# Optimization experiments

Hardware: AMD Instinct MI355X
Metric: run time of the kernel (lower is better)

Reference implementation:

```python
import jax, jax.numpy as jnp
import numpy as np

V, C, L, D = 16384, 16, 6, 64  # n_vars, max_clauses, max_variables, embedding_dim


def _normalize(x):
    # utils.normalize: L2-normalize along the feature axis
    return x / jnp.linalg.norm(x, axis=-1, keepdims=True)


def _rescombine(x, W1, b1, W2, b2):
    # ResidualCombine: normalize(sigmoid(layer1(x)) + layer2(x))
    h = jax.nn.sigmoid(x @ W1 + b1) + x @ W2 + b2
    return _normalize(h)


def setup_inputs() -> dict:
    key = jax.random.key(0)
    ks = jax.random.split(key, 14)
    s = 0.05
    variables = jax.random.normal(ks[0], (V, D), jnp.float32)
    # literal variable indices; slot 0 of every clause is the owning variable i
    lits = jax.random.randint(ks[1], (V, C, L), 0, V)
    lits = lits.at[:, :, 0].set(jnp.arange(V)[:, None])
    neg_mask = jax.random.bernoulli(ks[2], 0.5, (V, C, L))
    # literal validity: at least 2 literals per clause, slot 0 always valid
    nvar = jax.random.randint(ks[3], (V, C), 2, L + 1)
    var_valid = jnp.arange(L)[None, None, :] < nvar[:, :, None]
    # clause validity: at least 1 clause per variable
    nclause = jax.random.randint(ks[4], (V,), 1, C + 1)
    clause_valid = jnp.arange(C)[None, :] < nclause[:, None]
    # params
    Wn = jax.random.normal(ks[5], (D, D), jnp.float32) * s
    bn = jnp.zeros((D,), jnp.float32)
    f = jax.random.normal(ks[6], (D,), jnp.float32)
    false_emb = f / jnp.linalg.norm(f)  # Embedding(1, D, max_norm=1.0)
    W1v = jax.random.normal(ks[7], (L * D, D), jnp.float32) * s
    b1v = jnp.zeros((D,), jnp.float32)
    W2v = jax.random.normal(ks[8], (L * D, D), jnp.float32) * s
    b2v = jnp.zeros((D,), jnp.float32)
    W1c = jax.random.normal(ks[9], (C * D, D), jnp.float32) * s
    b1c = jnp.zeros((D,), jnp.float32)
    W2c = jax.random.normal(ks[10], (C * D, D), jnp.float32) * s
    b2c = jnp.zeros((D,), jnp.float32)
    return dict(variables=variables, lits=lits, neg_mask=neg_mask, var_valid=var_valid,
                clause_valid=clause_valid, Wn=Wn, bn=bn, false_emb=false_emb,
                W1v=W1v, b1v=b1v, W2v=W2v, b2v=b2v, W1c=W1c, b1c=b1c, W2c=W2c, b2c=b2c)


def reference(variables, lits, neg_mask, var_valid, clause_valid,
              Wn, bn, false_emb, W1v, b1v, W2v, b2v, W1c, b1c, W2c, b2c):
    # gather literal embeddings: [V, C, L, D]
    g = variables[lits]
    # negation linear for negative literals
    v = jnp.where(neg_mask[..., None], g @ Wn + bn, g)
    # pad invalid literal slots with the 'false' embedding
    v = jnp.where(var_valid[..., None], v, false_emb)
    # variable_combiner over flattened [L*D]
    clause_emb = _rescombine(v.reshape(V, C, L * D), W1v, b1v, W2v, b2v)  # [V, C, D]
    # pad missing clauses with 'true' = negation(false)
    true_emb = false_emb @ Wn + bn
    clause_emb = jnp.where(clause_valid[..., None], clause_emb, true_emb)
    # clause_combiner over flattened [C*D]
    out = _rescombine(clause_emb.reshape(V, C * D), W1c, b1c, W2c, b2c)  # [V, D]
    # variables with no clauses pass through unchanged
    has_clauses = clause_valid.any(axis=-1)
    return jnp.where(has_clauses[:, None], out, variables)
```

## Files before the change

kernel.cpp:

```cpp
#include <hip/hip_runtime.h>
#include <hip/hip_bf16.h>

#define NV 16384
#define NC 16
#define NL 6
#define ND 64

typedef unsigned short u16;
typedef unsigned int u32;
typedef __attribute__((ext_vector_type(8))) short short8;
typedef __attribute__((ext_vector_type(4))) float f32x4;

#define PB_BN  0
#define PB_FE  64
#define PB_B1V 128
#define PB_B2V 192
#define PB_B1C 256
#define PB_B2C 320
#define U_BVS   896
#define U_BCS   50048
#define U_BN    181120
#define U_VARSB 185216
#define U_NEGB  1233856
#define U_FIDX  2282496

__device__ __forceinline__ float ldbf(const u16* p, int i) {
  return __uint_as_float(((u32)p[i]) << 16);
}
__device__ __forceinline__ u16 f2b(float f) {
  u32 x = __float_as_uint(f);
  return (u16)((x + 0x7FFF + ((x >> 16) & 1)) >> 16);
}
__device__ __forceinline__ int ldmask(const void* p, int i, int bdt) {
  return bdt ? (int)((const signed char*)p)[i] : ((const int*)p)[i];
}
__device__ __forceinline__ float ldf(const void* p, int i, int fdt) {
  return fdt ? ldbf((const u16*)p, i) : ((const float*)p)[i];
}
__device__ __forceinline__ void gll16(const u16* g, u16* l) {
  __builtin_amdgcn_global_load_lds(
      (const __attribute__((address_space(1))) u32*)(g),
      (__attribute__((address_space(3))) u32*)(l), 16, 0, 0);
}

__global__ __launch_bounds__(256) void k_prep(
    const void* vars, const int* __restrict__ lits, const void* negm, const void* vval,
    const void* Wn, const void* bn, const void* femb,
    const void* W1v, const void* b1v, const void* W2v, const void* b2v,
    const void* W1c, const void* b1c, const void* W2c, const void* b2c,
    int* flags, float* pbuf, u16* wsB) {
  __shared__ int s_cnt[4], s_big[4];
  const int t = threadIdx.x;
  {
    const u32 w = ((const u32*)vars)[t];
    const u32 e = (w >> 7) & 0xFF;
    const unsigned long long bal = __ballot(e >= 0x6E && e <= 0x8E);
    const u32 bw = ((const u32*)vval)[t];
    const unsigned long long bb = __ballot(bw > 1u);
    if ((t & 63) == 0) { s_cnt[t >> 6] = __popcll(bal); s_big[t >> 6] = (bb != 0ull); }
  }
  __syncthreads();
  const int fdt = (s_cnt[0] + s_cnt[1] + s_cnt[2] + s_cnt[3]) >= 192;
  const int bdt = (s_big[0] | s_big[1] | s_big[2] | s_big[3]);
  const int bid = blockIdx.x;

  if (bid == 0) {
    if (t == 0) { flags[0] = fdt; flags[1] = bdt; }
    if (t < 64) {
      const void* src[6] = {bn, femb, b1v, b2v, b1c, b2c};
      const int off[6] = {PB_BN, PB_FE, PB_B1V, PB_B2V, PB_B1C, PB_B2C};
      for (int j = 0; j < 6; j++) pbuf[off[j] + t] = ldf(src[j], t, fdt);
      wsB[U_VARSB + NV * 64 + t] = fdt ? ((const u16*)femb)[t] : f2b(((const float*)femb)[t]);
    }
    for (int i = t; i < 4096; i += 256) {
      const int n = i >> 6, k = i & 63;
      wsB[U_BN + i] = f2b(ldf(Wn, k * 64 + n, fdt));
    }
  } else if (bid < 25) {
    const int c = (bid - 1) * 256 + t;
    const int ln = c & 63, nt = (c >> 6) & 7, ks = c >> 9;
    const int n = nt * 16 + (ln & 15);
    const void* src = (n < 64) ? W1v : W2v;
    const int kb = ks * 32 + (ln >> 4) * 8, n6 = n & 63;
    u16 o[8];
#pragma unroll
    for (int j = 0; j < 8; j++) o[j] = f2b(ldf(src, (kb + j) * 64 + n6, fdt));
    *(short8*)(wsB + U_BVS + c * 8) = *(short8*)o;
  } else if (bid < 89) {
    const int c = (bid - 25) * 256 + t;
    const int ln = c & 63, nt = (c >> 6) & 7, ks = c >> 9;
    const int n = nt * 16 + (ln & 15);
    const void* src = (n < 64) ? W1c : W2c;
    const int kb = ks * 32 + (ln >> 4) * 8, n6 = n & 63;
    u16 o[8];
#pragma unroll
    for (int j = 0; j < 8; j++) o[j] = f2b(ldf(src, (kb + j) * 64 + n6, fdt));
    *(short8*)(wsB + U_BCS + c * 8) = *(short8*)o;
  } else if (bid < 601) {
    const int c8 = (bid - 89) * 256 + t;
    u16 o[8];
    if (fdt) {
      *(short8*)o = ((const short8*)vars)[c8];
    } else {
      const float* f = (const float*)vars + c8 * 8;
#pragma unroll
      for (int j = 0; j < 8; j++) o[j] = f2b(f[j]);
    }
    *(short8*)(wsB + U_VARSB + c8 * 8) = *(short8*)o;
  } else {
    const int i0 = ((bid - 601) * 256 + t) * 4;
    u16 o[4];
#pragma unroll
    for (int j = 0; j < 4; j++) {
      const int i = i0 + j;
      const int valid = ldmask(vval, i, bdt);
      const int neg = ldmask(negm, i, bdt);
      const int idx = lits[i];
      o[j] = (u16)(valid ? (idx + (neg ? (NV + 1) : 0)) : NV);
    }
    *(ushort4*)(wsB + U_FIDX + i0) = *(ushort4*)o;
  }
}

__global__ __launch_bounds__(256) void k_negvar(const float* pbuf, u16* wsB) {
  const int tid = threadIdx.x, lane = tid & 63, wv = tid >> 6;
  const int col = lane & 15, quad = lane >> 4, q8 = quad * 8;
  const int rowbase = blockIdx.x * 64 + wv * 16;
  f32x4 acc[4];
#pragma unroll
  for (int nt = 0; nt < 4; nt++) acc[nt] = (f32x4){0.f, 0.f, 0.f, 0.f};
  const int arow = min(rowbase + col, NV);
#pragma unroll
  for (int ks = 0; ks < 2; ks++) {
    const short8 a = *(const short8*)(wsB + U_VARSB + arow * 64 + ks * 32 + q8);
#pragma unroll
    for (int nt = 0; nt < 4; nt++) {
      const short8 b = *(const short8*)(wsB + U_BN + (nt * 16 + col) * 64 + ks * 32 + q8);
      acc[nt] = __builtin_amdgcn_mfma_f32_16x16x32_bf16(a, b, acc[nt], 0, 0, 0);
    }
  }
#pragma unroll
  for (int reg = 0; reg < 4; reg++) {
    const int r = rowbase + quad * 4 + reg;
    if (r <= NV) {
#pragma unroll
      for (int nt = 0; nt < 4; nt++) {
        const int d = nt * 16 + col;
        wsB[U_NEGB + r * 64 + d] = f2b(acc[nt][reg] + pbuf[PB_BN + d]);
      }
    }
  }
}

__global__ __launch_bounds__(256, 2) void k_main(
    const void* __restrict__ vars, const void* __restrict__ cval,
    const float* __restrict__ pbuf, const int* __restrict__ flags,
    const u16* __restrict__ wsB, void* __restrict__ outv) {
  __shared__ __align__(16) u16 smem[24576];
  __shared__ float ps[16][4];
  __shared__ int hcS[16];

  const int tid = threadIdx.x, lane = tid & 63, wv = tid >> 6;
  const int col = lane & 15, quad = lane >> 4, q8 = quad * 8;
  const int fdt = flags[0], bdt = flags[1];
  const int vbase = (blockIdx.x * 4 + wv) * 4;
  const int v0 = blockIdx.x * 16;

  u32 r2_[4][3];
#pragma unroll
  for (int v4 = 0; v4 < 4; v4++)
#pragma unroll
    for (int i = 0; i < 3; i++)
      r2_[v4][i] = *(const u32*)(wsB + U_FIDX + (vbase + v4) * 96 + col * 6 + i * 2);

  const int cv = ldmask(cval, vbase * 16 + lane, bdt);
  const unsigned long long bal = __ballot(cv != 0);
  if (lane < 4) hcS[wv * 4 + lane] = ((bal >> (lane * 16)) & 0xFFFFull) != 0;

  f32x4 acc[4][8];
#pragma unroll
  for (int v4 = 0; v4 < 4; v4++)
#pragma unroll
    for (int nt = 0; nt < 8; nt++) acc[v4][nt] = (f32x4){0.f, 0.f, 0.f, 0.f};

#pragma unroll
  for (int j = 0; j < 6; j++) {
    const int cl = wv * 6 + j;
    gll16(wsB + U_BVS + cl * 512 + lane * 8, &smem[cl * 512]);
  }
  short8 a_cur[4], a_nxt[4];
#pragma unroll
  for (int v4 = 0; v4 < 4; v4++) {
    const int idx = (int)(r2_[v4][0] & 0xFFFFu);
    a_cur[v4] = *(const short8*)(wsB + U_VARSB + idx * 64 + q8);
  }
  __syncthreads();

  for (int q = 0; q < 4; q++) {
    if (q < 3) {
#pragma unroll
      for (int j = 0; j < 6; j++) {
        const int cl = wv * 6 + j;
        gll16(wsB + U_BVS + (q + 1) * 12288 + cl * 512 + lane * 8,
              &smem[((q + 1) & 1) * 12288 + cl * 512]);
      }
    }
#pragma unroll
    for (int ksl = 0; ksl < 3; ksl++) {
      const int gk = q * 3 + ksl;
      if (gk < 11) {
        const int gn = gk + 1;
        const int goff = (gn & 1) * 32 + q8;
        const int pi = gn >> 2, ph = (gn >> 1) & 1;
#pragma unroll
        for (int v4 = 0; v4 < 4; v4++) {
          const int idx = (int)((r2_[v4][pi] >> (ph * 16)) & 0xFFFFu);
          a_nxt[v4] = *(const short8*)(wsB + U_VARSB + idx * 64 + goff);
        }
      }
#pragma unroll
      for (int nt = 0; nt < 8; nt++) {
        const short8 b = *(const short8*)(&smem[(q & 1) * 12288 + (ksl * 8 + nt) * 512 + lane * 8]);
#pragma unroll
        for (int v4 = 0; v4 < 4; v4++)
          acc[v4][nt] = __builtin_amdgcn_mfma_f32_16x16x32_bf16(a_cur[v4], b, acc[v4][nt], 0, 0, 0);
      }
#pragma unroll
      for (int v4 = 0; v4 < 4; v4++) a_cur[v4] = a_nxt[v4];
    }
    if (q < 3) __syncthreads();
  }
  __syncthreads();

  {
    float b1l[4], b2l[4], truel[4];
#pragma unroll
    for (int nt = 0; nt < 4; nt++) {
      const int d = nt * 16 + col;
      b1l[nt] = pbuf[PB_B1V + d];
      b2l[nt] = pbuf[PB_B2V + d];
      truel[nt] = ldbf(wsB, U_NEGB + NV * 64 + d);
    }
#pragma unroll
    for (int v4 = 0; v4 < 4; v4++) {
      const u32 vmask = (u32)((bal >> (v4 * 16)) & 0xFFFFull);
      const int vloc = wv * 4 + v4;
#pragma unroll
      for (int reg = 0; reg < 4; reg++) {
        const int c = quad * 4 + reg;
        float hh[4], ss = 0.f;
#pragma unroll
        for (int nt = 0; nt < 4; nt++) {
          hh[nt] = 1.0f / (1.0f + __expf(-(acc[v4][nt][reg] + b1l[nt]))) + acc[v4][nt + 4][reg] + b2l[nt];
          ss += hh[nt] * hh[nt];
        }
        ss += __shfl_xor(ss, 1, 64); ss += __shfl_xor(ss, 2, 64);
        ss += __shfl_xor(ss, 4, 64); ss += __shfl_xor(ss, 8, 64);
        const float sc = 1.0f / sqrtf(ss);
        const int valid = (vmask >> c) & 1;
#pragma unroll
        for (int nt = 0; nt < 4; nt++) {
          const float o = valid ? hh[nt] * sc : truel[nt];
          const int l2 = (nt * 2 + (col >> 3)) & 3;
          smem[(c * 2 + (nt >> 1)) * 512 + (l2 * 16 + vloc) * 8 + (col & 7)] = f2b(o);
        }
      }
    }
  }
  __syncthreads();

  f32x4 acc1 = (f32x4){0.f, 0.f, 0.f, 0.f}, acc2 = (f32x4){0.f, 0.f, 0.f, 0.f};
#pragma unroll 8
  for (int ks = 0; ks < 32; ks++) {
    const short8 a = *(const short8*)(&smem[ks * 512 + lane * 8]);
    const short8 b1 = *(const short8*)(wsB + U_BCS + (ks * 8 + wv) * 512 + lane * 8);
    const short8 b2 = *(const short8*)(wsB + U_BCS + (ks * 8 + wv + 4) * 512 + lane * 8);
    acc1 = __builtin_amdgcn_mfma_f32_16x16x32_bf16(a, b1, acc1, 0, 0, 0);
    acc2 = __builtin_amdgcn_mfma_f32_16x16x32_bf16(a, b2, acc2, 0, 0, 0);
  }

  const int d = wv * 16 + col;
  const float b1c_d = pbuf[PB_B1C + d], b2c_d = pbuf[PB_B2C + d];
  float h[4];
#pragma unroll
  for (int reg = 0; reg < 4; reg++) {
    h[reg] = 1.0f / (1.0f + __expf(-(acc1[reg] + b1c_d))) + acc2[reg] + b2c_d;
    float ssp = h[reg] * h[reg];
    ssp += __shfl_xor(ssp, 1, 64); ssp += __shfl_xor(ssp, 2, 64);
    ssp += __shfl_xor(ssp, 4, 64); ssp += __shfl_xor(ssp, 8, 64);
    if (col == 0) ps[quad * 4 + reg][wv] = ssp;
  }
  __syncthreads();
#pragma unroll
  for (int reg = 0; reg < 4; reg++) {
    const int r = quad * 4 + reg;
    const float tot = ps[r][0] + ps[r][1] + ps[r][2] + ps[r][3];
    float o = h[reg] * (1.0f / sqrtf(tot));
    const int oi = (v0 + r) * 64 + d;
    if (hcS[r]) {
      if (fdt) ((u16*)outv)[oi] = f2b(o);
      else ((float*)outv)[oi] = o;
    } else {
      if (fdt) ((u16*)outv)[oi] = ((const u16*)vars)[oi];
      else ((float*)outv)[oi] = ((const float*)vars)[oi];
    }
  }
}

extern "C" void kernel_launch(void* const* d_in, const int* in_sizes, int n_in,
                              void* d_out, int out_size, void* d_ws, size_t ws_size,
                              hipStream_t stream) {
  const void* vars = d_in[0];
  const int* lits = (const int*)d_in[1];
  const void* negm = d_in[2];
  const void* vval = d_in[3];
  const void* cvalid = d_in[4];
  const void* Wn = d_in[5];
  const void* bn = d_in[6];
  const void* femb = d_in[7];
  const void* W1v = d_in[8];
  const void* b1v = d_in[9];
  const void* W2v = d_in[10];
  const void* b2v = d_in[11];
  const void* W1c = d_in[12];
  const void* b1c = d_in[13];
  const void* W2c = d_in[14];
  const void* b2c = d_in[15];

  int* flags = (int*)d_ws;
  float* pbuf = (float*)((char*)d_ws + 256);
  u16* wsB = (u16*)d_ws;

  k_prep<<<2137, 256, 0, stream>>>(vars, lits, negm, vval, Wn, bn, femb,
                                   W1v, b1v, W2v, b2v, W1c, b1c, W2c, b2c,
                                   flags, pbuf, wsB);
  k_negvar<<<(NV + 1 + 63) / 64, 256, 0, stream>>>(pbuf, wsB);
  k_main<<<NV / 16, 256, 0, stream>>>(vars, cvalid, pbuf, flags, wsB, d_out);
}
```

Before: 158.3 us.

## Fuse negation GEMM into prep kernel and halve variables per main block

Removes the separate negation-GEMM kernel by adding blocks to the prep kernel that build the transposed Wn in shared memory and read variables directly. The main kernel now processes 8 variables per block instead of 16, doubling the grid and reducing per-wave accumulator registers. This trades fewer launches and more parallelism/occupancy for halved reuse of the staged weight tiles and redundant Wn conversion per block.

```diff
diff --git a/kernel.cpp b/kernel.cpp
--- a/kernel.cpp
+++ b/kernel.cpp
@@ -19,7 +19,6 @@
 #define PB_B2C 320
 #define U_BVS   896
 #define U_BCS   50048
-#define U_BN    181120
 #define U_VARSB 185216
 #define U_NEGB  1233856
 #define U_FIDX  2282496
@@ -50,6 +49,7 @@
     const void* W1c, const void* b1c, const void* W2c, const void* b2c,
     int* flags, float* pbuf, u16* wsB) {
   __shared__ int s_cnt[4], s_big[4];
+  __shared__ __align__(16) u16 BnL[4096];
   const int t = threadIdx.x;
   {
     const u32 w = ((const u32*)vars)[t];
@@ -71,10 +71,6 @@
       const int off[6] = {PB_BN, PB_FE, PB_B1V, PB_B2V, PB_B1C, PB_B2C};
       for (int j = 0; j < 6; j++) pbuf[off[j] + t] = ldf(src[j], t, fdt);
       wsB[U_VARSB + NV * 64 + t] = fdt ? ((const u16*)femb)[t] : f2b(((const float*)femb)[t]);
-    }
-    for (int i = t; i < 4096; i += 256) {
-      const int n = i >> 6, k = i & 63;
-      wsB[U_BN + i] = f2b(ldf(Wn, k * 64 + n, fdt));
     }
   } else if (bid < 25) {
     const int c = (bid - 1) * 256 + t;
@@ -107,7 +103,7 @@
       for (int j = 0; j < 8; j++) o[j] = f2b(f[j]);
     }
     *(short8*)(wsB + U_VARSB + c8 * 8) = *(short8*)o;
-  } else {
+  } else if (bid < 2137) {
     const int i0 = ((bid - 601) * 256 + t) * 4;
     u16 o[4];
 #pragma unroll
@@ -119,67 +115,85 @@
       o[j] = (u16)(valid ? (idx + (neg ? (NV + 1) : 0)) : NV);
     }
     *(ushort4*)(wsB + U_FIDX + i0) = *(ushort4*)o;
-  }
-}
-
-__global__ __launch_bounds__(256) void k_negvar(const float* pbuf, u16* wsB) {
-  const int tid = threadIdx.x, lane = tid & 63, wv = tid >> 6;
-  const int col = lane & 15, quad = lane >> 4, q8 = quad * 8;
-  const int rowbase = blockIdx.x * 64 + wv * 16;
-  f32x4 acc[4];
-#pragma unroll
-  for (int nt = 0; nt < 4; nt++) acc[nt] = (f32x4){0.f, 0.f, 0.f, 0.f};
-  const int arow = min(rowbase + col, NV);
-#pragma unroll
-  for (int ks = 0; ks < 2; ks++) {
-    const short8 a = *(const short8*)(wsB + U_VARSB + arow * 64 + ks * 32 + q8);
-#pragma unroll
-    for (int nt = 0; nt < 4; nt++) {
-      const short8 b = *(const short8*)(wsB + U_BN + (nt * 16 + col) * 64 + ks * 32 + q8);
-      acc[nt] = __builtin_amdgcn_mfma_f32_16x16x32_bf16(a, b, acc[nt], 0, 0, 0);
-    }
-  }
-#pragma unroll
-  for (int reg = 0; reg < 4; reg++) {
-    const int r = rowbase + quad * 4 + reg;
-    if (r <= NV) {
+  } else {
+    const int lane = t & 63, wv = t >> 6;
+    const int col = lane & 15, quad = lane >> 4, q8 = quad * 8;
+    const int rowbase = (bid - 2137) * 64 + wv * 16;
+    for (int i = t; i < 4096; i += 256) {
+      const int n = i >> 6, k = i & 63;
+      BnL[i] = f2b(ldf(Wn, k * 64 + n, fdt));
+    }
+    __syncthreads();
+    const int arow = min(rowbase + col, NV);
+    short8 a[2];
+    if (fdt) {
+      const u16* src = (arow == NV) ? (const u16*)femb : (const u16*)vars + arow * 64;
+      a[0] = *(const short8*)(src + q8);
+      a[1] = *(const short8*)(src + 32 + q8);
+    } else {
+      const float* src = (arow == NV) ? (const float*)femb : (const float*)vars + arow * 64;
+      u16 tmp[16];
+#pragma unroll
+      for (int j = 0; j < 8; j++) tmp[j] = f2b(src[q8 + j]);
+#pragma unroll
+      for (int j = 0; j < 8; j++) tmp[8 + j] = f2b(src[32 + q8 + j]);
+      a[0] = *(short8*)tmp;
+      a[1] = *(short8*)(tmp + 8);
+    }
+    f32x4 acc[4];
+#pragma unroll
+    for (int nt = 0; nt < 4; nt++) acc[nt] = (f32x4){0.f, 0.f, 0.f, 0.f};
+#pragma unroll
+    for (int ks = 0; ks < 2; ks++) {
 #pragma unroll
       for (int nt = 0; nt < 4; nt++) {
-        const int d = nt * 16 + col;
-        wsB[U_NEGB + r * 64 + d] = f2b(acc[nt][reg] + pbuf[PB_BN + d]);
-      }
-    }
-  }
-}
-
-__global__ __launch_bounds__(256, 2) void k_main(
+        const short8 b = *(const short8*)(BnL + (nt * 16 + col) * 64 + ks * 32 + q8);
+        acc[nt] = __builtin_amdgcn_mfma_f32_16x16x32_bf16(a[ks], b, acc[nt], 0, 0, 0);
+      }
+    }
+#pragma unroll
+    for (int reg = 0; reg < 4; reg++) {
+      const int r = rowbase + quad * 4 + reg;
+      if (r <= NV) {
+#pragma unroll
+        for (int nt = 0; nt < 4; nt++) {
+          const int d = nt * 16 + col;
+          wsB[U_NEGB + r * 64 + d] = f2b(acc[nt][reg] + ldf(bn, d, fdt));
+        }
+      }
+    }
+  }
+}
+
+__global__ __launch_bounds__(256) void k_main(
     const void* __restrict__ vars, const void* __restrict__ cval,
     const float* __restrict__ pbuf, const int* __restrict__ flags,
     const u16* __restrict__ wsB, void* __restrict__ outv) {
   __shared__ __align__(16) u16 smem[24576];
   __shared__ float ps[16][4];
-  __shared__ int hcS[16];
+  __shared__ int hcS[8];
 
   const int tid = threadIdx.x, lane = tid & 63, wv = tid >> 6;
   const int col = lane & 15, quad = lane >> 4, q8 = quad * 8;
   const int fdt = flags[0], bdt = flags[1];
-  const int vbase = (blockIdx.x * 4 + wv) * 4;
-  const int v0 = blockIdx.x * 16;
-
-  u32 r2_[4][3];
-#pragma unroll
-  for (int v4 = 0; v4 < 4; v4++)
+  const int vbase = blockIdx.x * 8 + wv * 2;
+  const int v0 = blockIdx.x * 8;
+
+  u32 r2_[2][3];
+#pragma unroll
+  for (int v4 = 0; v4 < 2; v4++)
 #pragma unroll
     for (int i = 0; i < 3; i++)
       r2_[v4][i] = *(const u32*)(wsB + U_FIDX + (vbase + v4) * 96 + col * 6 + i * 2);
 
-  const int cv = ldmask(cval, vbase * 16 + lane, bdt);
+  int cv = 0;
+  if (lane < 32) cv = ldmask(cval, (vbase + (lane >> 4)) * NC + (lane & 15), bdt);
   const unsigned long long bal = __ballot(cv != 0);
-  if (lane < 4) hcS[wv * 4 + lane] = ((bal >> (lane * 16)) & 0xFFFFull) != 0;
-
-  f32x4 acc[4][8];
-#pragma unroll
-  for (int v4 = 0; v4 < 4; v4++)
+  if (lane < 2) hcS[wv * 2 + lane] = ((bal >> (lane * 16)) & 0xFFFFull) != 0;
+
+  f32x4 acc[2][8];
+#pragma unroll
+  for (int v4 = 0; v4 < 2; v4++)
 #pragma unroll
     for (int nt = 0; nt < 8; nt++) acc[v4][nt] = (f32x4){0.f, 0.f, 0.f, 0.f};
 
@@ -188,9 +202,9 @@
     const int cl = wv * 6 + j;
     gll16(wsB + U_BVS + cl * 512 + lane * 8, &smem[cl * 512]);
   }
-  short8 a_cur[4], a_nxt[4];
-#pragma unroll
-  for (int v4 = 0; v4 < 4; v4++) {
+  short8 a_cur[2], a_nxt[2];
+#pragma unroll
+  for (int v4 = 0; v4 < 2; v4++) {
     const int idx = (int)(r2_[v4][0] & 0xFFFFu);
     a_cur[v4] = *(const short8*)(wsB + U_VARSB + idx * 64 + q8);
   }
@@ -213,7 +227,7 @@
         const int goff = (gn & 1) * 32 + q8;
         const int pi = gn >> 2, ph = (gn >> 1) & 1;
 #pragma unroll
-        for (int v4 = 0; v4 < 4; v4++) {
+        for (int v4 = 0; v4 < 2; v4++) {
           const int idx = (int)((r2_[v4][pi] >> (ph * 16)) & 0xFFFFu);
           a_nxt[v4] = *(const short8*)(wsB + U_VARSB + idx * 64 + goff);
         }
@@ -222,11 +236,11 @@
       for (int nt = 0; nt < 8; nt++) {
         const short8 b = *(const short8*)(&smem[(q & 1) * 12288 + (ksl * 8 + nt) * 512 + lane * 8]);
 #pragma unroll
-        for (int v4 = 0; v4 < 4; v4++)
+        for (int v4 = 0; v4 < 2; v4++)
           acc[v4][nt] = __builtin_amdgcn_mfma_f32_16x16x32_bf16(a_cur[v4], b, acc[v4][nt], 0, 0, 0);
       }
 #pragma unroll
-      for (int v4 = 0; v4 < 4; v4++) a_cur[v4] = a_nxt[v4];
+      for (int v4 = 0; v4 < 2; v4++) a_cur[v4] = a_nxt[v4];
     }
     if (q < 3) __syncthreads();
   }
@@ -242,9 +256,9 @@
       truel[nt] = ldbf(wsB, U_NEGB + NV * 64 + d);
     }
 #pragma unroll
-    for (int v4 = 0; v4 < 4; v4++) {
+    for (int v4 = 0; v4 < 2; v4++) {
       const u32 vmask = (u32)((bal >> (v4 * 16)) & 0xFFFFull);
-      const int vloc = wv * 4 + v4;
+      const int vloc = wv * 2 + v4;
 #pragma unroll
       for (int reg = 0; reg < 4; reg++) {
         const int c = quad * 4 + reg;
@@ -294,15 +308,17 @@
 #pragma unroll
   for (int reg = 0; reg < 4; reg++) {
     const int r = quad * 4 + reg;
-    const float tot = ps[r][0] + ps[r][1] + ps[r][2] + ps[r][3];
-    float o = h[reg] * (1.0f / sqrtf(tot));
-    const int oi = (v0 + r) * 64 + d;
-    if (hcS[r]) {
-      if (fdt) ((u16*)outv)[oi] = f2b(o);
-      else ((float*)outv)[oi] = o;
-    } else {
-      if (fdt) ((u16*)outv)[oi] = ((const u16*)vars)[oi];
-      else ((float*)outv)[oi] = ((const float*)vars)[oi];
+    if (r < 8) {
+      const float tot = ps[r][0] + ps[r][1] + ps[r][2] + ps[r][3];
+      float o = h[reg] * (1.0f / sqrtf(tot));
+      const int oi = (v0 + r) * 64 + d;
+      if (hcS[r]) {
+        if (fdt) ((u16*)outv)[oi] = f2b(o);
+        else ((float*)outv)[oi] = o;
+      } else {
+        if (fdt) ((u16*)outv)[oi] = ((const u16*)vars)[oi];
+        else ((float*)outv)[oi] = ((const float*)vars)[oi];
+      }
     }
   }
 }
@@ -331,9 +347,8 @@
   float* pbuf = (float*)((char*)d_ws + 256);
   u16* wsB = (u16*)d_ws;
 
-  k_prep<<<2137, 256, 0, stream>>>(vars, lits, negm, vval, Wn, bn, femb,
+  k_prep<<<2394, 256, 0, stream>>>(vars, lits, negm, vval, Wn, bn, femb,
                                    W1v, b1v, W2v, b2v, W1c, b1c, W2c, b2c,
                                    flags, pbuf, wsB);
-  k_negvar<<<(NV + 1 + 63) / 64, 256, 0, stream>>>(pbuf, wsB);
-  k_main<<<NV / 16, 256, 0, stream>>>(vars, cvalid, pbuf, flags, wsB, d_out);
-}
+  k_main<<<NV / 8, 256, 0, stream>>>(vars, cvalid, pbuf, flags, wsB, d_out);
+}
```

New measurement: 177.5 us. 1.12x slower.

## Fold negation matmul into prep kernel and widen per-thread prep work

Applied to the files above, without the earlier changes.

Removes the separate k_negvar launch by computing the negated-variable table inside extra k_prep blocks. Each of those blocks transposes Wn into LDS and reads variables directly from the input instead of from the bf16 workspace copy. The variable-conversion and literal-index packing blocks now each handle 4x or 16x more elements per thread, using vectorized int4 loads, so the grid shrinks from 2137 to 858 blocks. This saves a kernel launch and the dependency between launches. In exchange, every neg block redundantly rebuilds the transposed Wn.

```diff
diff --git a/kernel.cpp b/kernel.cpp
--- a/kernel.cpp
+++ b/kernel.cpp
@@ -19,7 +19,6 @@
 #define PB_B2C 320
 #define U_BVS   896
 #define U_BCS   50048
-#define U_BN    181120
 #define U_VARSB 185216
 #define U_NEGB  1233856
 #define U_FIDX  2282496
@@ -50,6 +49,7 @@
     const void* W1c, const void* b1c, const void* W2c, const void* b2c,
     int* flags, float* pbuf, u16* wsB) {
   __shared__ int s_cnt[4], s_big[4];
+  __shared__ __align__(16) u16 BnL[4096];
   const int t = threadIdx.x;
   {
     const u32 w = ((const u32*)vars)[t];
@@ -71,10 +71,6 @@
       const int off[6] = {PB_BN, PB_FE, PB_B1V, PB_B2V, PB_B1C, PB_B2C};
       for (int j = 0; j < 6; j++) pbuf[off[j] + t] = ldf(src[j], t, fdt);
       wsB[U_VARSB + NV * 64 + t] = fdt ? ((const u16*)femb)[t] : f2b(((const float*)femb)[t]);
-    }
-    for (int i = t; i < 4096; i += 256) {
-      const int n = i >> 6, k = i & 63;
-      wsB[U_BN + i] = f2b(ldf(Wn, k * 64 + n, fdt));
     }
   } else if (bid < 25) {
     const int c = (bid - 1) * 256 + t;
@@ -96,57 +92,91 @@
 #pragma unroll
     for (int j = 0; j < 8; j++) o[j] = f2b(ldf(src, (kb + j) * 64 + n6, fdt));
     *(short8*)(wsB + U_BCS + c * 8) = *(short8*)o;
+  } else if (bid < 217) {
+    const int c8 = ((bid - 89) * 256 + t) * 4;
+#pragma unroll
+    for (int cc = 0; cc < 4; cc++) {
+      u16 o[8];
+      if (fdt) {
+        *(short8*)o = ((const short8*)vars)[c8 + cc];
+      } else {
+        const float* f = (const float*)vars + (c8 + cc) * 8;
+#pragma unroll
+        for (int j = 0; j < 8; j++) o[j] = f2b(f[j]);
+      }
+      *(short8*)(wsB + U_VARSB + (c8 + cc) * 8) = *(short8*)o;
+    }
   } else if (bid < 601) {
-    const int c8 = (bid - 89) * 256 + t;
-    u16 o[8];
+    const int i0 = ((bid - 217) * 256 + t) * 16;
+    u16 o[16];
+    if (!bdt) {
+      const int4* lp = (const int4*)(lits + i0);
+      const int4* vp = (const int4*)((const int*)vval + i0);
+      const int4* np = (const int4*)((const int*)negm + i0);
+#pragma unroll
+      for (int c4 = 0; c4 < 4; c4++) {
+        const int4 L = lp[c4], V = vp[c4], N = np[c4];
+        o[c4 * 4 + 0] = (u16)(V.x ? (L.x + (N.x ? (NV + 1) : 0)) : NV);
+        o[c4 * 4 + 1] = (u16)(V.y ? (L.y + (N.y ? (NV + 1) : 0)) : NV);
+        o[c4 * 4 + 2] = (u16)(V.z ? (L.z + (N.z ? (NV + 1) : 0)) : NV);
+        o[c4 * 4 + 3] = (u16)(V.w ? (L.w + (N.w ? (NV + 1) : 0)) : NV);
+      }
+    } else {
+#pragma unroll
+      for (int j = 0; j < 16; j++) {
+        const int i = i0 + j;
+        const int valid = ldmask(vval, i, bdt);
+        const int neg = ldmask(negm, i, bdt);
+        o[j] = (u16)(valid ? (lits[i] + (neg ? (NV + 1) : 0)) : NV);
+      }
+    }
+    *(short8*)(wsB + U_FIDX + i0) = *(short8*)o;
+    *(short8*)(wsB + U_FIDX + i0 + 8) = *(short8*)(o + 8);
+  } else {
+    const int lane = t & 63, wv = t >> 6;
+    const int col = lane & 15, quad = lane >> 4, q8 = quad * 8;
+    const int rowbase = (bid - 601) * 64 + wv * 16;
+    for (int i = t; i < 4096; i += 256) {
+      const int n = i >> 6, k = i & 63;
+      BnL[i] = f2b(ldf(Wn, k * 64 + n, fdt));
+    }
+    __syncthreads();
+    const int arow = min(rowbase + col, NV);
+    short8 a[2];
     if (fdt) {
-      *(short8*)o = ((const short8*)vars)[c8];
+      const u16* src = (arow == NV) ? (const u16*)femb : (const u16*)vars + arow * 64;
+      a[0] = *(const short8*)(src + q8);
+      a[1] = *(const short8*)(src + 32 + q8);
     } else {
-      const float* f = (const float*)vars + c8 * 8;
-#pragma unroll
-      for (int j = 0; j < 8; j++) o[j] = f2b(f[j]);
-    }
-    *(short8*)(wsB + U_VARSB + c8 * 8) = *(short8*)o;
-  } else {
-    const int i0 = ((bid - 601) * 256 + t) * 4;
-    u16 o[4];
-#pragma unroll
-    for (int j = 0; j < 4; j++) {
-      const int i = i0 + j;
-      const int valid = ldmask(vval, i, bdt);
-      const int neg = ldmask(negm, i, bdt);
-      const int idx = lits[i];
-      o[j] = (u16)(valid ? (idx + (neg ? (NV + 1) : 0)) : NV);
-    }
-    *(ushort4*)(wsB + U_FIDX + i0) = *(ushort4*)o;
-  }
-}
-
-__global__ __launch_bounds__(256) void k_negvar(const float* pbuf, u16* wsB) {
-  const int tid = threadIdx.x, lane = tid & 63, wv = tid >> 6;
-  const int col = lane & 15, quad = lane >> 4, q8 = quad * 8;
-  const int rowbase = blockIdx.x * 64 + wv * 16;
-  f32x4 acc[4];
-#pragma unroll
-  for (int nt = 0; nt < 4; nt++) acc[nt] = (f32x4){0.f, 0.f, 0.f, 0.f};
-  const int arow = min(rowbase + col, NV);
-#pragma unroll
-  for (int ks = 0; ks < 2; ks++) {
-    const short8 a = *(const short8*)(wsB + U_VARSB + arow * 64 + ks * 32 + q8);
-#pragma unroll
-    for (int nt = 0; nt < 4; nt++) {
-      const short8 b = *(const short8*)(wsB + U_BN + (nt * 16 + col) * 64 + ks * 32 + q8);
-      acc[nt] = __builtin_amdgcn_mfma_f32_16x16x32_bf16(a, b, acc[nt], 0, 0, 0);
-    }
-  }
-#pragma unroll
-  for (int reg = 0; reg < 4; reg++) {
-    const int r = rowbase + quad * 4 + reg;
-    if (r <= NV) {
+      const float* src = (arow == NV) ? (const float*)femb : (const float*)vars + arow * 64;
+      u16 tmp[16];
+#pragma unroll
+      for (int j = 0; j < 8; j++) tmp[j] = f2b(src[q8 + j]);
+#pragma unroll
+      for (int j = 0; j < 8; j++) tmp[8 + j] = f2b(src[32 + q8 + j]);
+      a[0] = *(short8*)tmp;
+      a[1] = *(short8*)(tmp + 8);
+    }
+    f32x4 acc[4];
+#pragma unroll
+    for (int nt = 0; nt < 4; nt++) acc[nt] = (f32x4){0.f, 0.f, 0.f, 0.f};
+#pragma unroll
+    for (int ks = 0; ks < 2; ks++) {
 #pragma unroll
       for (int nt = 0; nt < 4; nt++) {
-        const int d = nt * 16 + col;
-        wsB[U_NEGB + r * 64 + d] = f2b(acc[nt][reg] + pbuf[PB_BN + d]);
+        const short8 b = *(const short8*)(BnL + (nt * 16 + col) * 64 + ks * 32 + q8);
+        acc[nt] = __builtin_amdgcn_mfma_f32_16x16x32_bf16(a[ks], b, acc[nt], 0, 0, 0);
+      }
+    }
+#pragma unroll
+    for (int reg = 0; reg < 4; reg++) {
+      const int r = rowbase + quad * 4 + reg;
+      if (r <= NV) {
+#pragma unroll
+        for (int nt = 0; nt < 4; nt++) {
+          const int d = nt * 16 + col;
+          wsB[U_NEGB + r * 64 + d] = f2b(acc[nt][reg] + ldf(bn, d, fdt));
+        }
       }
     }
   }
@@ -331,9 +361,8 @@
   float* pbuf = (float*)((char*)d_ws + 256);
   u16* wsB = (u16*)d_ws;
 
-  k_prep<<<2137, 256, 0, stream>>>(vars, lits, negm, vval, Wn, bn, femb,
-                                   W1v, b1v, W2v, b2v, W1c, b1c, W2c, b2c,
-                                   flags, pbuf, wsB);
-  k_negvar<<<(NV + 1 + 63) / 64, 256, 0, stream>>>(pbuf, wsB);
+  k_prep<<<858, 256, 0, stream>>>(vars, lits, negm, vval, Wn, bn, femb,
+                                  W1v, b1v, W2v, b2v, W1c, b1c, W2c, b2c,
+                                  flags, pbuf, wsB);
   k_main<<<NV / 16, 256, 0, stream>>>(vars, cvalid, pbuf, flags, wsB, d_out);
 }
```

After: 159.4 us. About the same (+0.7%).
